# Performance work log

Hardware: AMD Instinct MI355X
Metric: run time of the kernel (lower is better)

## Reference

```python
import jax, jax.numpy as jnp
import numpy as np

MD = 40                 # max_displacement
K = 2 * MD + 1          # 81 kernel size -> K*K = 6561 displacements


def setup_inputs() -> dict:
    key = jax.random.key(0)
    k1, k2 = jax.random.split(key)
    b, c, h, w = 2, 128, 64, 96
    x1 = jax.random.normal(k1, (b, c, h, w), dtype=jnp.float32)
    x2 = jax.random.normal(k2, (b, c, h, w), dtype=jnp.float32)
    return {"x1": x1, "x2": x2}


def reference(x1, x2):
    b, c, h, w = x1.shape
    # zero-pad x2 by MD on each spatial side (matches F.pad(x2, (pad,)*4))
    x2p = jnp.pad(x2, ((0, 0), (0, 0), (MD, MD), (MD, MD)))

    # Fused sliding-window correlation: scan over the K*K displacements,
    # slicing a (b,c,h,w) window of x2p and reducing over channels.
    # Avoids the (b,c,K^2,h,w) unfold blow-up entirely.
    def step(carry, s):
        dy = s // K
        dx = s % K
        win = jax.lax.dynamic_slice(x2p, (0, 0, dy, dx), (b, c, h, w))
        return carry, jnp.einsum('bchw,bchw->bhw', x1, win)

    _, corr = jax.lax.scan(step, None, jnp.arange(K * K))  # (K*K, b, h, w)
    corr = jnp.transpose(corr, (1, 0, 2, 3))               # (b, K*K, h, w)
    return corr / jnp.sqrt(jnp.float32(c))
```

## Files before the change

kernel.cpp:

```cpp
#include <hip/hip_runtime.h>

#define CH    128
#define HH    64
#define WW    96
#define MD    40
#define KD    81
#define HW    (HH*WW)
#define CHW   (CH*HW)
#define SCALE 0.08838834764831845f
#define LSTR  72
#define CHUNK (WW*LSTR)
#define WS2_USH ((size_t)2*HH*2*CHUNK)
#define NWG   (HH*KD*2)

typedef __attribute__((ext_vector_type(8))) short bf16x8;
typedef __attribute__((ext_vector_type(4))) float f32x4;

__device__ inline unsigned int pack2bf(float lo, float hi) {
    unsigned int a = __float_as_uint(lo), b = __float_as_uint(hi);
    a = (a + 0x7FFFu + ((a >> 16) & 1u)) >> 16;
    b = (b + 0x7FFFu + ((b >> 16) & 1u)) >> 16;
    return a | (b << 16);
}

__device__ __forceinline__ void gload16(const void* g, void* l) {
    __builtin_amdgcn_global_load_lds(
        (const __attribute__((address_space(1))) void*)g,
        (__attribute__((address_space(3))) void*)l, 16, 0, 0);
}

__global__ __launch_bounds__(256) void prepack(
    const float* __restrict__ x1, const float* __restrict__ x2,
    unsigned short* __restrict__ ws)
{
    const int y = blockIdx.x;
    const int h = blockIdx.y & 1;
    const int t = blockIdx.y >> 1;
    const int b = blockIdx.z;

    const float* src = (t ? x2 : x1)
        + (size_t)b * CHW + (size_t)(h * 64) * HW + (size_t)y * WW;
    unsigned short* dst = ws + (size_t)t * WS2_USH
        + ((size_t)(b * HH + y) * 2 + h) * CHUNK;

    for (int j = threadIdx.x; j < 8 * WW; j += 256) {
        const int cg = j / WW;
        const int x  = j - cg * WW;
        const float* p = src + (size_t)(cg * 8) * HW + x;
        float f[8];
        #pragma unroll
        for (int i = 0; i < 8; ++i) f[i] = p[(size_t)i * HW];
        uint4 w;
        w.x = pack2bf(f[0], f[1]); w.y = pack2bf(f[2], f[3]);
        w.z = pack2bf(f[4], f[5]); w.w = pack2bf(f[6], f[7]);
        *reinterpret_cast<uint4*>(&dst[(size_t)x * LSTR + cg * 8]) = w;
    }
}

__device__ __forceinline__ void mfma_half(
    const unsigned short* sA, const unsigned short* sB,
    int m0, int n0, int lr, int q, f32x4 (&acc)[3][3])
{
    #pragma unroll
    for (int kk = 0; kk < 2; ++kk) {
        const int cl = kk * 32 + q * 8;
        bf16x8 af[3], bg[3];
        #pragma unroll
        for (int i = 0; i < 3; ++i)
            af[i] = *reinterpret_cast<const bf16x8*>(&sB[(m0 + 16 * i + lr) * LSTR + cl]);
        #pragma unroll
        for (int j = 0; j < 3; ++j)
            bg[j] = *reinterpret_cast<const bf16x8*>(&sA[(n0 + 16 * j + lr) * LSTR + cl]);
        #pragma unroll
        for (int i = 0; i < 3; ++i)
            #pragma unroll
            for (int j = 0; j < 3; ++j)
                acc[i][j] = __builtin_amdgcn_mfma_f32_16x16x32_bf16(
                    af[i], bg[j], acc[i][j], 0, 0, 0);
    }
}

__global__ __launch_bounds__(256, 4) void corr_kernel(
    const unsigned short* __restrict__ ws, float* __restrict__ out)
{
    const int wg  = blockIdx.x;
    const int b   = (wg >= HH * KD) ? 1 : 0;
    const int rem = wg - b * (HH * KD);
    const int dy  = rem >> 6;
    const int y   = rem & 63;
    const int tid = threadIdx.x;

    float* outbase = out + ((size_t)b * (KD * KD) + (size_t)dy * KD) * HW
                         + (size_t)y * WW;

    const int y2 = y + dy - MD;
    if (y2 < 0 || y2 >= HH) {
        const float4 z = make_float4(0.f, 0.f, 0.f, 0.f);
        #pragma unroll
        for (int it = 0; it < 8; ++it) {
            const int idx = it * 256 + tid;
            if (idx < KD * (WW / 4)) {
                const int dx = idx / 24;
                const int x4 = idx - dx * 24;
                *reinterpret_cast<float4*>(outbase + (size_t)dx * HW + x4 * 4) = z;
            }
        }
        return;
    }

    __shared__ __align__(16) char smem[KD * WW * 4];
    unsigned short* sStage = reinterpret_cast<unsigned short*>(smem);
    unsigned short* sA = sStage;
    unsigned short* sB = sStage + CHUNK;
    float*          sG = reinterpret_cast<float*>(smem);

    const unsigned short* wsA = ws + ((size_t)(b * HH + y ) * 2) * CHUNK;
    const unsigned short* wsB = ws + WS2_USH + ((size_t)(b * HH + y2) * 2) * CHUNK;

    const int lane = tid & 63;
    const int wave = tid >> 6;
    const int m0   = (wave >> 1) * 48;
    const int n0   = (wave & 1) * 48;
    const int lr   = lane & 15;
    const int q    = lane >> 4;

    f32x4 acc[3][3];
    #pragma unroll
    for (int i = 0; i < 3; ++i)
        #pragma unroll
        for (int j = 0; j < 3; ++j)
            acc[i][j] = (f32x4){0.f, 0.f, 0.f, 0.f};

    for (int h = 0; h < 2; ++h) {
        if (h) __syncthreads();
        const unsigned short* g1 = wsA + (size_t)h * CHUNK;
        const unsigned short* g2 = wsB + (size_t)h * CHUNK;
        #pragma unroll
        for (int it = 0; it < 7; ++it) {
            const int idx = it * 256 + tid;
            if (idx < 2 * (CHUNK / 8)) {
                const unsigned short* g = (idx < (CHUNK / 8))
                    ? g1 + (size_t)idx * 8
                    : g2 + (size_t)(idx - (CHUNK / 8)) * 8;
                gload16(g, sStage + (size_t)idx * 8);
            }
        }
        __syncthreads();

        mfma_half(sA, sB, m0, n0, lr, q, acc);
    }

    __syncthreads();
    #pragma unroll
    for (int i = 0; i < 3; ++i) {
        #pragma unroll
        for (int j = 0; j < 3; ++j) {
            const int col  = n0 + 16 * j + lr;
            const int rowb = m0 + 16 * i + q * 4;
            #pragma unroll
            for (int r = 0; r < 4; ++r) {
                const int dxv = (rowb + r) - col + MD;
                if ((unsigned)dxv < (unsigned)KD) {
                    const int w = (dxv * WW + col) ^ (((dxv >> 2) & 1) << 4);
                    sG[w] = acc[i][j][r] * SCALE;
                }
            }
        }
    }
    __syncthreads();

    int dx = tid / 24;
    int x  = 4 * tid - dx * WW;
    #pragma unroll
    for (int it = 0; it < 8; ++it) {
        if (it < 7 || tid < 152) {
            const int baddr = ((dx * WW + x) << 2) ^ (((dx >> 2) & 1) << 6);
            float4 v = *reinterpret_cast<const float4*>(smem + baddr);
            const int x2b = x + dx - MD;
            v.x = ((unsigned)(x2b + 0) < (unsigned)WW) ? v.x : 0.f;
            v.y = ((unsigned)(x2b + 1) < (unsigned)WW) ? v.y : 0.f;
            v.z = ((unsigned)(x2b + 2) < (unsigned)WW) ? v.z : 0.f;
            v.w = ((unsigned)(x2b + 3) < (unsigned)WW) ? v.w : 0.f;
            *reinterpret_cast<float4*>(outbase + (size_t)(dx * HW + x)) = v;
        }
        x += 64; dx += 10;
        if (x >= WW) { x -= WW; ++dx; }
    }
}

extern "C" void kernel_launch(void* const* d_in, const int* in_sizes, int n_in,
                              void* d_out, int out_size, void* d_ws, size_t ws_size,
                              hipStream_t stream) {
    const float* x1 = (const float*)d_in[0];
    const float* x2 = (const float*)d_in[1];
    float* out = (float*)d_out;
    unsigned short* ws = (unsigned short*)d_ws;

    hipLaunchKernelGGL(prepack, dim3(HH, 4, 2), dim3(256), 0, stream, x1, x2, ws);

    hipLaunchKernelGGL(corr_kernel, dim3(NWG), dim3(256), 0, stream, ws, out);
}
```

Baseline: 339.8 us.

## Load MFMA operands directly from global memory, drop LDS staging

The correlation kernel now reads bf16 operand fragments straight from the prepacked global workspace into registers, instead of staging both chunks through LDS with global_load_lds. This removes the staging loads and two barriers per workgroup. The packed row stride shrinks from 72 to 64 since LDS bank padding is no longer needed. Operand reuse now depends on L1/L2 caching: each wave reloads its fragments from global memory, so latency is exposed with no barrier-separated prefetch.

```diff
diff --git a/kernel.cpp b/kernel.cpp
--- a/kernel.cpp
+++ b/kernel.cpp
@@ -8,7 +8,7 @@
 #define HW    (HH*WW)
 #define CHW   (CH*HW)
 #define SCALE 0.08838834764831845f
-#define LSTR  72
+#define LSTR  64
 #define CHUNK (WW*LSTR)
 #define WS2_USH ((size_t)2*HH*2*CHUNK)
 #define NWG   (HH*KD*2)
@@ -21,12 +21,6 @@
     a = (a + 0x7FFFu + ((a >> 16) & 1u)) >> 16;
     b = (b + 0x7FFFu + ((b >> 16) & 1u)) >> 16;
     return a | (b << 16);
-}
-
-__device__ __forceinline__ void gload16(const void* g, void* l) {
-    __builtin_amdgcn_global_load_lds(
-        (const __attribute__((address_space(1))) void*)g,
-        (__attribute__((address_space(3))) void*)l, 16, 0, 0);
 }
 
 __global__ __launch_bounds__(256) void prepack(
@@ -54,29 +48,6 @@
         w.x = pack2bf(f[0], f[1]); w.y = pack2bf(f[2], f[3]);
         w.z = pack2bf(f[4], f[5]); w.w = pack2bf(f[6], f[7]);
         *reinterpret_cast<uint4*>(&dst[(size_t)x * LSTR + cg * 8]) = w;
-    }
-}
-
-__device__ __forceinline__ void mfma_half(
-    const unsigned short* sA, const unsigned short* sB,
-    int m0, int n0, int lr, int q, f32x4 (&acc)[3][3])
-{
-    #pragma unroll
-    for (int kk = 0; kk < 2; ++kk) {
-        const int cl = kk * 32 + q * 8;
-        bf16x8 af[3], bg[3];
-        #pragma unroll
-        for (int i = 0; i < 3; ++i)
-            af[i] = *reinterpret_cast<const bf16x8*>(&sB[(m0 + 16 * i + lr) * LSTR + cl]);
-        #pragma unroll
-        for (int j = 0; j < 3; ++j)
-            bg[j] = *reinterpret_cast<const bf16x8*>(&sA[(n0 + 16 * j + lr) * LSTR + cl]);
-        #pragma unroll
-        for (int i = 0; i < 3; ++i)
-            #pragma unroll
-            for (int j = 0; j < 3; ++j)
-                acc[i][j] = __builtin_amdgcn_mfma_f32_16x16x32_bf16(
-                    af[i], bg[j], acc[i][j], 0, 0, 0);
     }
 }
 
@@ -109,10 +80,7 @@
     }
 
     __shared__ __align__(16) char smem[KD * WW * 4];
-    unsigned short* sStage = reinterpret_cast<unsigned short*>(smem);
-    unsigned short* sA = sStage;
-    unsigned short* sB = sStage + CHUNK;
-    float*          sG = reinterpret_cast<float*>(smem);
+    float* sG = reinterpret_cast<float*>(smem);
 
     const unsigned short* wsA = ws + ((size_t)(b * HH + y ) * 2) * CHUNK;
     const unsigned short* wsB = ws + WS2_USH + ((size_t)(b * HH + y2) * 2) * CHUNK;
@@ -131,26 +99,29 @@
         for (int j = 0; j < 3; ++j)
             acc[i][j] = (f32x4){0.f, 0.f, 0.f, 0.f};
 
+    #pragma unroll
     for (int h = 0; h < 2; ++h) {
-        if (h) __syncthreads();
-        const unsigned short* g1 = wsA + (size_t)h * CHUNK;
-        const unsigned short* g2 = wsB + (size_t)h * CHUNK;
+        const unsigned short* pA = wsA + (size_t)h * CHUNK;
+        const unsigned short* pB = wsB + (size_t)h * CHUNK;
         #pragma unroll
-        for (int it = 0; it < 7; ++it) {
-            const int idx = it * 256 + tid;
-            if (idx < 2 * (CHUNK / 8)) {
-                const unsigned short* g = (idx < (CHUNK / 8))
-                    ? g1 + (size_t)idx * 8
-                    : g2 + (size_t)(idx - (CHUNK / 8)) * 8;
-                gload16(g, sStage + (size_t)idx * 8);
-            }
+        for (int kk = 0; kk < 2; ++kk) {
+            const int cl = kk * 32 + q * 8;
+            bf16x8 af[3], bg[3];
+            #pragma unroll
+            for (int i = 0; i < 3; ++i)
+                af[i] = *reinterpret_cast<const bf16x8*>(&pB[(m0 + 16 * i + lr) * LSTR + cl]);
+            #pragma unroll
+            for (int j = 0; j < 3; ++j)
+                bg[j] = *reinterpret_cast<const bf16x8*>(&pA[(n0 + 16 * j + lr) * LSTR + cl]);
+            #pragma unroll
+            for (int i = 0; i < 3; ++i)
+                #pragma unroll
+                for (int j = 0; j < 3; ++j)
+                    acc[i][j] = __builtin_amdgcn_mfma_f32_16x16x32_bf16(
+                        af[i], bg[j], acc[i][j], 0, 0, 0);
         }
-        __syncthreads();
-
-        mfma_half(sA, sB, m0, n0, lr, q, acc);
     }
 
-    __syncthreads();
     #pragma unroll
     for (int i = 0; i < 3; ++i) {
         #pragma unroll
```

New measurement: 374.8 us. 1.1x slower.
